# Kernel tuning notes

Hardware: AMD Instinct MI355X
Metric: run time of the kernel (lower is better)

The kernel has to match this reference:

```python
import jax, jax.numpy as jnp
import numpy as np

BLOCKSIZE = 128
KEEPER = 128


def setup_inputs() -> dict:
    key = jax.random.key(0)
    ks = jax.random.split(key, 8)
    S, H = 2048, 4096
    n_nonout = H - KEEPER          # 3968
    nb = n_nonout // BLOCKSIZE     # 31 low-precision blocks
    return {
        "x": jax.random.normal(ks[0], (1, S, H), dtype=jnp.float32),
        "weight": jax.random.normal(ks[1], (H, H), dtype=jnp.float32),   # [out, in]
        "scales": jax.random.uniform(ks[2], (H, n_nonout), dtype=jnp.float32),
        "keep_scales": jax.random.uniform(ks[3], (H, 1), dtype=jnp.float32),
        "inp_scales_lo": jax.random.uniform(ks[4], (S, nb), dtype=jnp.float32),
        "inp_scales_hi": jax.random.uniform(ks[5], (S, 1), dtype=jnp.float32),
        "inp_base_lo": jax.random.uniform(ks[6], (S, nb), dtype=jnp.float32),
        "inp_base_hi": jax.random.uniform(ks[7], (S, 1), dtype=jnp.float32),
    }


def reference(x, weight, scales, keep_scales, inp_scales_lo, inp_scales_hi,
              inp_base_lo, inp_base_hi):
    # Faithful vectorization of QLinearLayer._forward (channel_group == 0, bias None).
    bs, S, H = x.shape
    xs = x[0]                      # [S, H]  (bs == 1 assert in original)
    W = weight.T                   # [H, O]
    n_nonout = H - KEEPER
    nb = n_nonout // BLOCKSIZE
    O = W.shape[1]

    # Per-block weight scales: scales[:, i1] for each block start i1 -> [nb, O]
    w_blk_scales = scales[:, 0:n_nonout:BLOCKSIZE].T              # [nb, O]

    # Blockwise outer-product scaling fused into the operands:
    # y[s,o] = sum_n sc_lo[s,n] * ws[n,o] * (x_block_n @ W_block_n)[s,o]
    x_lo = xs[:, :n_nonout].reshape(S, nb, BLOCKSIZE) * inp_scales_lo[:, :, None]
    W_lo = W[:n_nonout, :].reshape(nb, BLOCKSIZE, O) * w_blk_scales[:, None, :]
    y = x_lo.reshape(S, n_nonout) @ W_lo.reshape(n_nonout, O)     # [S, O]

    # int8 keeper channels (high-precision path)
    hi_scales = inp_scales_hi @ keep_scales.T                      # [S, O]
    y_hi = xs[:, n_nonout:] @ W[n_nonout:, :]                      # [S, O]
    y = y + y_hi * hi_scales

    return y.reshape(bs, S, O)
```

## Files before the change

kernel.cpp:

```cpp
#include <hip/hip_runtime.h>

#define S_DIM 2048
#define K_DIM 4096
#define O_DIM 4096
#define NNON  3968
#define NB    31

#define XBLK 8192
#define WBLK 16384

typedef __bf16 bf16x8 __attribute__((ext_vector_type(8)));
typedef float  f32x4  __attribute__((ext_vector_type(4)));

__device__ __forceinline__ unsigned short f2bf(float f) {
    union { float f; unsigned u; } v; v.f = f;
    unsigned r = v.u + 0x7FFFu + ((v.u >> 16) & 1u);
    return (unsigned short)(r >> 16);
}

__global__ __launch_bounds__(256) void prepass(const float* __restrict__ x,
                                               const float* __restrict__ sc_lo,
                                               const float* __restrict__ sc_hi,
                                               const float* __restrict__ w,
                                               const float* __restrict__ scales,
                                               const float* __restrict__ keep,
                                               unsigned short* __restrict__ A,
                                               unsigned short* __restrict__ B)
{
    const int b = blockIdx.x;
    if (b < XBLK) {
        int idx = b * 256 + threadIdx.x;
        int s = idx >> 10;
        int k = (idx & 1023) << 2;
        float4 v = ((const float4*)x)[idx];
        float sc = (k < NNON) ? sc_lo[s * NB + (k >> 7)] : sc_hi[s];
        ushort4 o;
        o.x = f2bf(v.x * sc); o.y = f2bf(v.y * sc);
        o.z = f2bf(v.z * sc); o.w = f2bf(v.w * sc);
        ((ushort4*)A)[idx] = o;
    } else {
        int idx = (b - XBLK) * 256 + threadIdx.x;
        int o = idx >> 10;
        int k = (idx & 1023) << 2;
        float4 v = ((const float4*)w)[idx];
        float sc = (k < NNON) ? scales[(size_t)o * NNON + ((k >> 7) << 7)] : keep[o];
        ushort4 r;
        r.x = f2bf(v.x * sc); r.y = f2bf(v.y * sc);
        r.z = f2bf(v.z * sc); r.w = f2bf(v.w * sc);
        ((ushort4*)B)[idx] = r;
    }
}

#define BM 128
#define BN 128
#define BK 128

__global__ __launch_bounds__(256, 2) void gemm_bt(const unsigned short* __restrict__ A,
                                                  const unsigned short* __restrict__ B,
                                                  float* __restrict__ C)
{
    __shared__ unsigned short As[BM * BK];
    __shared__ unsigned short Bs[BN * BK];

    const int tid  = threadIdx.x;
    const int wave = tid >> 6;
    const int lane = tid & 63;
    const int quad = lane >> 4;
    const int l16  = lane & 15;
    const int bm = blockIdx.y * BM;
    const int bn = blockIdx.x * BN;
    const int wm = (wave >> 1) * 64;
    const int wn = (wave & 1) * 64;

    const int srow4 = lane >> 4;
    const int c16   = lane & 15;

    const unsigned short* Ab = A + (size_t)(bm + wave * 32 + srow4) * K_DIM;
    const unsigned short* Bb = B + (size_t)(bn + wave * 32 + srow4) * K_DIM;

    f32x4 acc[4][4];
    #pragma unroll
    for (int i = 0; i < 4; ++i)
        #pragma unroll
        for (int j = 0; j < 4; ++j)
            acc[i][j] = (f32x4){0.f, 0.f, 0.f, 0.f};

    auto stage = [&](int k0) {
        #pragma unroll
        for (int c = 0; c < 8; ++c) {
            const int gc = ((c16 ^ ((c * 4 + srow4) & 15)) << 3);
            __builtin_amdgcn_global_load_lds(
                (__attribute__((address_space(1))) unsigned int*)(Ab + (size_t)(c * 4) * K_DIM + k0 + gc),
                (__attribute__((address_space(3))) unsigned int*)(&As[(wave * 32 + c * 4) * BK]),
                16, 0, 0);
            __builtin_amdgcn_global_load_lds(
                (__attribute__((address_space(1))) unsigned int*)(Bb + (size_t)(c * 4) * K_DIM + k0 + gc),
                (__attribute__((address_space(3))) unsigned int*)(&Bs[(wave * 32 + c * 4) * BK]),
                16, 0, 0);
        }
    };

    stage(0);
    __syncthreads();

    for (int k0 = 0; k0 < K_DIM; k0 += BK) {
        bf16x8 af[4][4], bfr[4][4];
        #pragma unroll
        for (int ks = 0; ks < 4; ++ks) {
            #pragma unroll
            for (int i = 0; i < 4; ++i)
                af[ks][i] = *(const bf16x8*)(&As[(wm + i * 16 + l16) * BK + (((ks * 4 + quad) ^ l16) << 3)]);
            #pragma unroll
            for (int j = 0; j < 4; ++j)
                bfr[ks][j] = *(const bf16x8*)(&Bs[(wn + j * 16 + l16) * BK + (((ks * 4 + quad) ^ l16) << 3)]);
        }
        __syncthreads();

        if (k0 + BK < K_DIM)
            stage(k0 + BK);

        #pragma unroll
        for (int ks = 0; ks < 4; ++ks)
            #pragma unroll
            for (int i = 0; i < 4; ++i)
                #pragma unroll
                for (int j = 0; j < 4; ++j)
                    acc[i][j] = __builtin_amdgcn_mfma_f32_16x16x32_bf16(af[ks][i], bfr[ks][j], acc[i][j], 0, 0, 0);

        __syncthreads();
    }

    #pragma unroll
    for (int i = 0; i < 4; ++i)
        #pragma unroll
        for (int j = 0; j < 4; ++j) {
            const int col = bn + wn + j * 16 + l16;
            #pragma unroll
            for (int r = 0; r < 4; ++r) {
                const int row = bm + wm + i * 16 + quad * 4 + r;
                C[(size_t)row * O_DIM + col] = acc[i][j][r];
            }
        }
}

extern "C" void kernel_launch(void* const* d_in, const int* in_sizes, int n_in,
                              void* d_out, int out_size, void* d_ws, size_t ws_size,
                              hipStream_t stream) {
    const float* x      = (const float*)d_in[0];
    const float* weight = (const float*)d_in[1];
    const float* scales = (const float*)d_in[2];
    const float* keep   = (const float*)d_in[3];
    const float* sc_lo  = (const float*)d_in[4];
    const float* sc_hi  = (const float*)d_in[5];

    unsigned short* A = (unsigned short*)d_ws;
    unsigned short* B = A + (size_t)S_DIM * K_DIM;

    prepass<<<XBLK + WBLK, 256, 0, stream>>>(x, sc_lo, sc_hi, weight, scales, keep, A, B);

    dim3 grid(O_DIM / BN, S_DIM / BM);
    gemm_bt<<<grid, 256, 0, stream>>>(A, B, (float*)d_out);
}
```

Baseline: 243.4 us.

## Double-buffer GEMM with 128x256 tiles, split barriers and swizzled block order

Rewrites the bf16 GEMM main loop to use a two-stage LDS double buffer with 128x256 tiles, BK=64 and 512 threads (8 waves). Global-to-LDS loads are issued two tiles ahead and gated by explicit vmcnt waits and raw s_barrier instead of __syncthreads. The A and B loads are split into separate phases, and MFMA blocks are raised in priority so loads overlap compute. A block-index remap is added to improve L2 locality. LDS use rises to 96KB per block, which may limit occupancy, and the hand-written waitcnt logic is fragile.

```diff
diff --git a/kernel.cpp b/kernel.cpp
--- a/kernel.cpp
+++ b/kernel.cpp
@@ -52,31 +52,46 @@
 }
 
 #define BM 128
-#define BN 128
-#define BK 128
-
-__global__ __launch_bounds__(256, 2) void gemm_bt(const unsigned short* __restrict__ A,
+#define BN 256
+#define BK 64
+#define NT (K_DIM / BK)
+
+#define GPTR(p) ((__attribute__((address_space(1))) unsigned int*)(p))
+#define LPTR(p) ((__attribute__((address_space(3))) unsigned int*)(p))
+
+__device__ __forceinline__ void vm_wait6() { asm volatile("s_waitcnt vmcnt(6)" ::: "memory"); }
+__device__ __forceinline__ void vm_wait0() { asm volatile("s_waitcnt vmcnt(0)" ::: "memory"); }
+__device__ __forceinline__ void wg_barrier() {
+    asm volatile("" ::: "memory");
+    __builtin_amdgcn_s_barrier();
+    asm volatile("" ::: "memory");
+}
+
+__global__ __launch_bounds__(512, 2) void gemm_bt(const unsigned short* __restrict__ A,
                                                   const unsigned short* __restrict__ B,
                                                   float* __restrict__ C)
 {
-    __shared__ unsigned short As[BM * BK];
-    __shared__ unsigned short Bs[BN * BK];
+    __shared__ __align__(16) unsigned short As[2][BM * BK];
+    __shared__ __align__(16) unsigned short Bs[2][BN * BK];
 
     const int tid  = threadIdx.x;
     const int wave = tid >> 6;
     const int lane = tid & 63;
     const int quad = lane >> 4;
     const int l16  = lane & 15;
-    const int bm = blockIdx.y * BM;
-    const int bn = blockIdx.x * BN;
-    const int wm = (wave >> 1) * 64;
-    const int wn = (wave & 1) * 64;
-
-    const int srow4 = lane >> 4;
-    const int c16   = lane & 15;
-
-    const unsigned short* Ab = A + (size_t)(bm + wave * 32 + srow4) * K_DIM;
-    const unsigned short* Bb = B + (size_t)(bn + wave * 32 + srow4) * K_DIM;
+
+    const int wg = blockIdx.x;
+    const int sw = (wg & 7) * 32 + (wg >> 3);
+    const int bm = (sw >> 4) * BM;
+    const int bn = (sw & 15) * BN;
+
+    const int wm = (wave >> 2) * 64;
+    const int wn = (wave & 3) * 64;
+
+    const int r8 = lane >> 3;
+    const int q8 = lane & 7;
+    const unsigned short* Ag = A + (size_t)(bm + wave * 8 + r8) * K_DIM + ((q8 ^ r8) << 3);
+    const unsigned short* Bg = B + (size_t)(bn + wave * 8 + r8) * K_DIM + ((q8 ^ r8) << 3);
 
     f32x4 acc[4][4];
     #pragma unroll
@@ -85,49 +100,82 @@
         for (int j = 0; j < 4; ++j)
             acc[i][j] = (f32x4){0.f, 0.f, 0.f, 0.f};
 
-    auto stage = [&](int k0) {
-        #pragma unroll
-        for (int c = 0; c < 8; ++c) {
-            const int gc = ((c16 ^ ((c * 4 + srow4) & 15)) << 3);
-            __builtin_amdgcn_global_load_lds(
-                (__attribute__((address_space(1))) unsigned int*)(Ab + (size_t)(c * 4) * K_DIM + k0 + gc),
-                (__attribute__((address_space(3))) unsigned int*)(&As[(wave * 32 + c * 4) * BK]),
-                16, 0, 0);
-            __builtin_amdgcn_global_load_lds(
-                (__attribute__((address_space(1))) unsigned int*)(Bb + (size_t)(c * 4) * K_DIM + k0 + gc),
-                (__attribute__((address_space(3))) unsigned int*)(&Bs[(wave * 32 + c * 4) * BK]),
-                16, 0, 0);
+    auto stageA = [&](int t) {
+        unsigned short* dst = &As[t & 1][wave * 8 * BK];
+        #pragma unroll
+        for (int s = 0; s < 2; ++s)
+            __builtin_amdgcn_global_load_lds(GPTR(Ag + (size_t)(s * 64) * K_DIM + t * BK),
+                                             LPTR(dst + s * 64 * BK), 16, 0, 0);
+    };
+    auto stageB = [&](int t) {
+        unsigned short* dst = &Bs[t & 1][wave * 8 * BK];
+        #pragma unroll
+        for (int s = 0; s < 4; ++s)
+            __builtin_amdgcn_global_load_lds(GPTR(Bg + (size_t)(s * 64) * K_DIM + t * BK),
+                                             LPTR(dst + s * 64 * BK), 16, 0, 0);
+    };
+
+    stageA(0); stageB(0);
+    stageA(1); stageB(1);
+    vm_wait6();
+    wg_barrier();
+
+    #pragma unroll 2
+    for (int t = 0; t < NT; ++t) {
+        const int cur = t & 1;
+        const unsigned short* asb = As[cur];
+        const unsigned short* bsb = Bs[cur];
+
+        bf16x8 af[2][4], b01[2][2];
+        #pragma unroll
+        for (int ks = 0; ks < 2; ++ks) {
+            #pragma unroll
+            for (int i = 0; i < 4; ++i)
+                af[ks][i] = *(const bf16x8*)&asb[(wm + i * 16 + l16) * BK +
+                                                 (((ks * 4 + quad) ^ (l16 & 7)) << 3)];
+            #pragma unroll
+            for (int j = 0; j < 2; ++j)
+                b01[ks][j] = *(const bf16x8*)&bsb[(wn + j * 16 + l16) * BK +
+                                                  (((ks * 4 + quad) ^ (l16 & 7)) << 3)];
         }
-    };
-
-    stage(0);
-    __syncthreads();
-
-    for (int k0 = 0; k0 < K_DIM; k0 += BK) {
-        bf16x8 af[4][4], bfr[4][4];
-        #pragma unroll
-        for (int ks = 0; ks < 4; ++ks) {
-            #pragma unroll
-            for (int i = 0; i < 4; ++i)
-                af[ks][i] = *(const bf16x8*)(&As[(wm + i * 16 + l16) * BK + (((ks * 4 + quad) ^ l16) << 3)]);
-            #pragma unroll
-            for (int j = 0; j < 4; ++j)
-                bfr[ks][j] = *(const bf16x8*)(&Bs[(wn + j * 16 + l16) * BK + (((ks * 4 + quad) ^ l16) << 3)]);
-        }
-        __syncthreads();
-
-        if (k0 + BK < K_DIM)
-            stage(k0 + BK);
-
-        #pragma unroll
-        for (int ks = 0; ks < 4; ++ks)
+        wg_barrier();
+        if (t < NT - 2) stageA(t + 2);
+
+        __builtin_amdgcn_s_setprio(1);
+        #pragma unroll
+        for (int ks = 0; ks < 2; ++ks)
             #pragma unroll
             for (int i = 0; i < 4; ++i)
                 #pragma unroll
-                for (int j = 0; j < 4; ++j)
-                    acc[i][j] = __builtin_amdgcn_mfma_f32_16x16x32_bf16(af[ks][i], bfr[ks][j], acc[i][j], 0, 0, 0);
-
-        __syncthreads();
+                for (int j = 0; j < 2; ++j)
+                    acc[i][j] = __builtin_amdgcn_mfma_f32_16x16x32_bf16(af[ks][i], b01[ks][j],
+                                                                        acc[i][j], 0, 0, 0);
+        __builtin_amdgcn_s_setprio(0);
+
+        bf16x8 b23[2][2];
+        #pragma unroll
+        for (int ks = 0; ks < 2; ++ks)
+            #pragma unroll
+            for (int j = 0; j < 2; ++j)
+                b23[ks][j] = *(const bf16x8*)&bsb[(wn + (j + 2) * 16 + l16) * BK +
+                                                  (((ks * 4 + quad) ^ (l16 & 7)) << 3)];
+        wg_barrier();
+        if (t < NT - 2) stageB(t + 2);
+
+        __builtin_amdgcn_s_setprio(1);
+        #pragma unroll
+        for (int ks = 0; ks < 2; ++ks)
+            #pragma unroll
+            for (int i = 0; i < 4; ++i)
+                #pragma unroll
+                for (int j = 0; j < 2; ++j)
+                    acc[i][j + 2] = __builtin_amdgcn_mfma_f32_16x16x32_bf16(af[ks][i], b23[ks][j],
+                                                                            acc[i][j + 2], 0, 0, 0);
+        __builtin_amdgcn_s_setprio(0);
+
+        if (t < NT - 2)       vm_wait6();
+        else if (t == NT - 2) vm_wait0();
+        wg_barrier();
     }
 
     #pragma unroll
@@ -158,6 +206,6 @@
 
     prepass<<<XBLK + WBLK, 256, 0, stream>>>(x, sc_lo, sc_hi, weight, scales, keep, A, B);
 
-    dim3 grid(O_DIM / BN, S_DIM / BM);
-    gemm_bt<<<grid, 256, 0, stream>>>(A, B, (float*)d_out);
-}
+    dim3 grid(256);
+    gemm_bt<<<grid, 512, 0, stream>>>(A, B, (float*)d_out);
+}
```

New measurement: 245.2 us. Within noise of the previous version (+0.8%).
